# Kernel tuning notes

Measured on AMD Instinct MI355X. Metric: run time of the kernel, lower is better.

Reference implementation:

```python
import jax, jax.numpy as jnp
import numpy as np

P = 2.0  # exponent from init kwarg p


def _segment_mean(vals, idx, n):
    # scatter-mean with zero for empty segments (matches torch_scatter reduce='mean')
    s = jax.ops.segment_sum(vals, idx, num_segments=n)
    c = jax.ops.segment_sum(jnp.ones((vals.shape[0], 1), vals.dtype), idx, num_segments=n)
    return s / jnp.maximum(c, 1.0)


def setup_inputs() -> dict:
    key = jax.random.key(0)
    ks = jax.random.split(key, 6)
    N, E, nhid, heads = 100000, 3200000, 64, 4
    X = jax.random.normal(ks[0], (N, nhid), dtype=jnp.float32)
    edge_index = jax.random.randint(ks[1], (2, E), 0, N, dtype=jnp.int32)
    s1 = 1.0 / np.sqrt(nhid)
    W_self = jax.random.normal(ks[2], (nhid, nhid), dtype=jnp.float32) * s1
    W_neigh = jax.random.normal(ks[3], (nhid, nhid), dtype=jnp.float32) * s1
    b_conv = jnp.zeros((nhid,), dtype=jnp.float32)
    s2 = 1.0 / np.sqrt(2 * nhid)
    Qw = jax.random.normal(ks[4], (heads, 2 * nhid, nhid // heads), dtype=jnp.float32) * s2
    Qb = jnp.zeros((heads, nhid // heads), dtype=jnp.float32)
    return {"X": X, "edge_index": edge_index, "W_self": W_self,
            "W_neigh": W_neigh, "b_conv": b_conv, "Qw": Qw, "Qb": Qb}


def reference(X, edge_index, W_self, W_neigh, b_conv, Qw, Qb):
    N = X.shape[0]
    src, dst = edge_index[0], edge_index[1]
    # GraphSAGE conv: self-linear + linear over mean of neighbor features, then ReLU
    agg = _segment_mean(X[src], dst, N)                     # [N, nhid]
    X2 = jax.nn.relu(X @ W_self + agg @ W_neigh + b_conv)   # [N, nhid]
    # gather both edge endpoints and concat
    ef = jnp.concatenate([X2[src], X2[dst]], axis=1)        # [E, 2*nhid]
    # per-head small linear, abs^p, heads concatenated -> [E, nhid]
    h = jnp.einsum('ef,hfd->ehd', ef, Qw) + Qb              # [E, heads, nhid/heads]
    h = (jnp.abs(h) ** P).reshape(ef.shape[0], -1)
    # scatter-mean by source node, tanh
    gg = jnp.tanh(_segment_mean(h, src, N))                 # [N, nhid]
    return gg
```

## Files before the change

### kernel.cpp

```cpp
#include <hip/hip_runtime.h>
#include <math.h>

#define NHID 64
#define NPB 512
#define NPB_SHIFT 9
#define MAXB 256
#define CAP 20480
#define CHUNK 8192

__device__ __forceinline__ float bf_lo(unsigned u) { return __uint_as_float(u << 16); }
__device__ __forceinline__ float bf_hi(unsigned u) { return __uint_as_float(u & 0xffff0000u); }
__device__ __forceinline__ unsigned f2bf(float f) {
    unsigned u = __float_as_uint(f);
    return (u + 0x7fffu + ((u >> 16) & 1u)) >> 16;
}

__global__ __launch_bounds__(256) void k_build(const int* __restrict__ src,
                                               const int* __restrict__ dst,
                                               unsigned int* __restrict__ buf0,
                                               unsigned int* __restrict__ buf1,
                                               int* __restrict__ btail0,
                                               int* __restrict__ btail1,
                                               const float* __restrict__ X,
                                               unsigned* __restrict__ Xb,
                                               const float* __restrict__ Qw,
                                               float* __restrict__ W2,
                                               int E, int nB, int nBucketBlocks,
                                               int nXcastBlocks, int N) {
    __shared__ int h[MAXB], b[MAXB];
    __shared__ int sk[CHUNK];
    int bid = blockIdx.x;
    int tid = threadIdx.x;

    if (bid >= nBucketBlocks) {
        int xb = bid - nBucketBlocks;
        if (xb < nXcastBlocks) {
            int i = xb * 256 + tid;
            if (i < N * 8) {
                const float4* Xv = (const float4*)X;
                float4 f0 = Xv[(size_t)i * 2];
                float4 f1 = Xv[(size_t)i * 2 + 1];
                uint4 p;
                p.x = f2bf(f0.x) | (f2bf(f0.y) << 16);
                p.y = f2bf(f0.z) | (f2bf(f0.w) << 16);
                p.z = f2bf(f1.x) | (f2bf(f1.y) << 16);
                p.w = f2bf(f1.z) | (f2bf(f1.w) << 16);
                ((uint4*)Xb)[i] = p;
            }
        } else {
            int i = (xb - nXcastBlocks) * 256 + tid;
            if (i < 8192) {
                int f = i >> 7, c = i & 127;
                float v;
                if (c < 64) v = Qw[(c >> 4) * 2048 + f * 16 + (c & 15)];
                else { int cc = c - 64; v = Qw[(cc >> 4) * 2048 + (64 + f) * 16 + (cc & 15)]; }
                W2[i] = v;
            }
        }
        return;
    }

    int side  = bid & 1;
    int chunk = bid >> 1;
    const int* key = side ? src : dst;
    const int* pay = side ? dst : src;
    unsigned int* buf = side ? buf1 : buf0;
    int* btail = side ? btail1 : btail0;

    for (int i = tid; i < nB; i += 256) h[i] = 0;
    __syncthreads();
    int e0 = chunk * CHUNK;
    for (int i = tid; i < CHUNK / 4; i += 256) {
        int e = e0 + i * 4;
        int4 k4;
        if (e + 3 < E) {
            k4 = ((const int4*)(key + e0))[i];
            atomicAdd(&h[k4.x >> NPB_SHIFT], 1);
            atomicAdd(&h[k4.y >> NPB_SHIFT], 1);
            atomicAdd(&h[k4.z >> NPB_SHIFT], 1);
            atomicAdd(&h[k4.w >> NPB_SHIFT], 1);
        } else {
            k4.x = (e     < E) ? key[e]     : 0;
            k4.y = (e + 1 < E) ? key[e + 1] : 0;
            k4.z = (e + 2 < E) ? key[e + 2] : 0;
            k4.w = (e + 3 < E) ? key[e + 3] : 0;
            if (e     < E) atomicAdd(&h[k4.x >> NPB_SHIFT], 1);
            if (e + 1 < E) atomicAdd(&h[k4.y >> NPB_SHIFT], 1);
            if (e + 2 < E) atomicAdd(&h[k4.z >> NPB_SHIFT], 1);
            if (e + 3 < E) atomicAdd(&h[k4.w >> NPB_SHIFT], 1);
        }
        ((int4*)sk)[i] = k4;
    }
    __syncthreads();
    for (int i = tid; i < nB; i += 256) {
        int c = h[i];
        b[i] = c ? atomicAdd(&btail[i], c) : 0;
        h[i] = 0;
    }
    __syncthreads();
    for (int i = tid; i < CHUNK / 4; i += 256) {
        int e = e0 + i * 4;
        int4 k4 = ((const int4*)sk)[i];
        if (e + 3 < E) {
            int4 p4 = ((const int4*)(pay + e0))[i];
            int bb, r;
            bb = k4.x >> NPB_SHIFT; r = atomicAdd(&h[bb], 1) + b[bb];
            if (r < CAP) buf[(size_t)bb * CAP + r] = ((unsigned)p4.x << NPB_SHIFT) | (unsigned)(k4.x & (NPB - 1));
            bb = k4.y >> NPB_SHIFT; r = atomicAdd(&h[bb], 1) + b[bb];
            if (r < CAP) buf[(size_t)bb * CAP + r] = ((unsigned)p4.y << NPB_SHIFT) | (unsigned)(k4.y & (NPB - 1));
            bb = k4.z >> NPB_SHIFT; r = atomicAdd(&h[bb], 1) + b[bb];
            if (r < CAP) buf[(size_t)bb * CAP + r] = ((unsigned)p4.z << NPB_SHIFT) | (unsigned)(k4.z & (NPB - 1));
            bb = k4.w >> NPB_SHIFT; r = atomicAdd(&h[bb], 1) + b[bb];
            if (r < CAP) buf[(size_t)bb * CAP + r] = ((unsigned)p4.w << NPB_SHIFT) | (unsigned)(k4.w & (NPB - 1));
        } else {
            int ks[4] = {k4.x, k4.y, k4.z, k4.w};
            for (int j = 0; j < 4; ++j) {
                int e2 = e + j;
                if (e2 < E) {
                    int k = ks[j], p = pay[e2];
                    int bb = k >> NPB_SHIFT;
                    int r = atomicAdd(&h[bb], 1) + b[bb];
                    if (r < CAP) buf[(size_t)bb * CAP + r] = ((unsigned)p << NPB_SHIFT) | (unsigned)(k & (NPB - 1));
                }
            }
        }
    }
}

__global__ __launch_bounds__(256) void k_bscan(const int* __restrict__ btail0,
                                               const int* __restrict__ btail1,
                                               int* __restrict__ boff0, int* __restrict__ boff1,
                                               int* __restrict__ off0, int* __restrict__ off1,
                                               int nB, int N) {
    __shared__ int sd[256];
    int tid = threadIdx.x;
    int v = (tid < nB) ? min(btail0[tid], CAP) : 0;
    sd[tid] = v; __syncthreads();
    for (int o = 1; o < 256; o <<= 1) {
        int t = (tid >= o) ? sd[tid - o] : 0; __syncthreads();
        sd[tid] += t; __syncthreads();
    }
    if (tid < nB) boff0[tid] = sd[tid] - v;
    if (tid == 255) off0[N] = sd[255];
    __syncthreads();
    v = (tid < nB) ? min(btail1[tid], CAP) : 0;
    sd[tid] = v; __syncthreads();
    for (int o = 1; o < 256; o <<= 1) {
        int t = (tid >= o) ? sd[tid - o] : 0; __syncthreads();
        sd[tid] += t; __syncthreads();
    }
    if (tid < nB) boff1[tid] = sd[tid] - v;
    if (tid == 255) off1[N] = sd[255];
}

__device__ void csr_work(const unsigned int* __restrict__ bufb, int cnt_b, int boff,
                         int* __restrict__ off, int* __restrict__ csr,
                         int N, int bucket) {
    __shared__ int cnt[NPB];
    __shared__ int scn[NPB];
    __shared__ int cur[NPB];
    int tid = threadIdx.x;
    cnt[tid] = 0;
    __syncthreads();
    for (int i = tid; i < cnt_b; i += 512)
        atomicAdd(&cnt[bufb[i] & (NPB - 1)], 1);
    __syncthreads();
    int v = cnt[tid];
    scn[tid] = v; __syncthreads();
    for (int o = 1; o < 512; o <<= 1) {
        int t = (tid >= o) ? scn[tid - o] : 0; __syncthreads();
        scn[tid] += t; __syncthreads();
    }
    int base = boff + scn[tid] - v;
    cur[tid] = base;
    int node = (bucket << NPB_SHIFT) + tid;
    if (node < N) off[node] = base;
    __syncthreads();
    for (int i = tid; i < cnt_b; i += 512) {
        unsigned int u = bufb[i];
        int pos = atomicAdd(&cur[u & (NPB - 1)], 1);
        csr[pos] = (int)(u >> NPB_SHIFT);
    }
}

__global__ __launch_bounds__(512) void k_csr0(const unsigned int* __restrict__ buf0,
                                              const int* __restrict__ btail0,
                                              const int* __restrict__ boff0,
                                              int* __restrict__ off0,
                                              int* __restrict__ csr0, int N) {
    int b = blockIdx.x;
    csr_work(buf0 + (size_t)b * CAP, min(btail0[b], CAP), boff0[b], off0, csr0, N, b);
}

#define AGG_ACC(u) \
    accA.x += bf_lo(u.x); accA.y += bf_hi(u.x); \
    accA.z += bf_lo(u.y); accA.w += bf_hi(u.y); \
    accB.x += bf_lo(u.z); accB.y += bf_hi(u.z); \
    accB.z += bf_lo(u.w); accB.w += bf_hi(u.w);
#define AGG_ACCM(u, f) \
    accA.x += f * bf_lo(u.x); accA.y += f * bf_hi(u.x); \
    accA.z += f * bf_lo(u.y); accA.w += f * bf_hi(u.y); \
    accB.x += f * bf_lo(u.z); accB.y += f * bf_hi(u.z); \
    accB.z += f * bf_lo(u.w); accB.w += f * bf_hi(u.w);

__global__ __launch_bounds__(512) void k_aggcsr(const unsigned* __restrict__ Xb,
                                                const int* __restrict__ off_dst,
                                                const int* __restrict__ csr_dst,
                                                unsigned* __restrict__ aggb,
                                                const unsigned int* __restrict__ buf1,
                                                const int* __restrict__ btail1,
                                                const int* __restrict__ boff1,
                                                int* __restrict__ off1,
                                                int* __restrict__ csr1,
                                                int N, int nB) {
    int bid = blockIdx.x;
    if (bid < nB) {
        csr_work(buf1 + (size_t)bid * CAP, min(btail1[bid], CAP), boff1[bid],
                 off1, csr1, N, bid);
        return;
    }
    int abid = bid - nB;
    int tid = threadIdx.x;
    int lane = tid & 63;
    int node = abid * 8 + (tid >> 6);
    if (node >= N) return;
    int grp = lane >> 3, col8 = lane & 7;
    const uint4* Xb4 = (const uint4*)Xb;
    int s0 = off_dst[node], s1 = off_dst[node + 1];
    float4 accA = make_float4(0.f, 0.f, 0.f, 0.f);
    float4 accB = make_float4(0.f, 0.f, 0.f, 0.f);
    for (int base = s0; base < s1; base += 64) {
        int cnt = min(64, s1 - base);
        int idx = (base + lane < s1) ? csr_dst[base + lane] : 0;
        int j = 0;
        for (; j + 32 <= cnt; j += 32) {
            int m0 = __shfl(idx, j + grp);
            int m1 = __shfl(idx, j + 8 + grp);
            int m2 = __shfl(idx, j + 16 + grp);
            int m3 = __shfl(idx, j + 24 + grp);
            uint4 u0 = Xb4[(size_t)m0 * 8 + col8];
            uint4 u1 = Xb4[(size_t)m1 * 8 + col8];
            uint4 u2 = Xb4[(size_t)m2 * 8 + col8];
            uint4 u3 = Xb4[(size_t)m3 * 8 + col8];
            AGG_ACC(u0); AGG_ACC(u1); AGG_ACC(u2); AGG_ACC(u3);
        }
        if (j < cnt) {
            int q0 = j + grp, q1 = j + 8 + grp, q2 = j + 16 + grp, q3 = j + 24 + grp;
            int m0 = __shfl(idx, q0);
            int m1 = __shfl(idx, q1);
            int m2 = __shfl(idx, q2);
            int m3 = __shfl(idx, q3);
            float f0 = (q0 < cnt) ? 1.f : 0.f; if (q0 >= cnt) m0 = 0;
            float f1 = (q1 < cnt) ? 1.f : 0.f; if (q1 >= cnt) m1 = 0;
            float f2 = (q2 < cnt) ? 1.f : 0.f; if (q2 >= cnt) m2 = 0;
            float f3 = (q3 < cnt) ? 1.f : 0.f; if (q3 >= cnt) m3 = 0;
            uint4 u0 = Xb4[(size_t)m0 * 8 + col8];
            uint4 u1 = Xb4[(size_t)m1 * 8 + col8];
            uint4 u2 = Xb4[(size_t)m2 * 8 + col8];
            uint4 u3 = Xb4[(size_t)m3 * 8 + col8];
            AGG_ACCM(u0, f0); AGG_ACCM(u1, f1); AGG_ACCM(u2, f2); AGG_ACCM(u3, f3);
        }
    }
    #pragma unroll
    for (int d = 8; d < 64; d <<= 1) {
        accA.x += __shfl_xor(accA.x, d); accA.y += __shfl_xor(accA.y, d);
        accA.z += __shfl_xor(accA.z, d); accA.w += __shfl_xor(accA.w, d);
        accB.x += __shfl_xor(accB.x, d); accB.y += __shfl_xor(accB.y, d);
        accB.z += __shfl_xor(accB.z, d); accB.w += __shfl_xor(accB.w, d);
    }
    if (grp == 0) {
        int deg = s1 - s0;
        float inv = 1.f / (float)max(deg, 1);
        uint4 p;
        p.x = f2bf(accA.x * inv) | (f2bf(accA.y * inv) << 16);
        p.y = f2bf(accA.z * inv) | (f2bf(accA.w * inv) << 16);
        p.z = f2bf(accB.x * inv) | (f2bf(accB.y * inv) << 16);
        p.w = f2bf(accB.z * inv) | (f2bf(accB.w * inv) << 16);
        ((uint4*)aggb)[(size_t)node * 8 + col8] = p;
    }
}

__global__ __launch_bounds__(256) void k_phaseA(const unsigned* __restrict__ Xb,
                                                const unsigned* __restrict__ aggb,
                                                const float* __restrict__ Ws,
                                                const float* __restrict__ Wn,
                                                const float* __restrict__ bconv,
                                                unsigned* __restrict__ X2b, int N) {
    __shared__ float sWs[4096];
    __shared__ float sWn[4096];
    __shared__ float sb[64];
    int tid = threadIdx.x;
    for (int i = tid; i < 4096; i += 256) {
        sWs[i] = Ws[i];
        sWn[i] = Wn[i];
    }
    if (tid < 64) sb[tid] = bconv[tid];
    __syncthreads();

    int n = blockIdx.x * 64 + (tid >> 2);
    if (n >= N) return;
    int wb = (tid & 3) << 2;
    const float4* ws4 = (const float4*)sWs;
    const float4* wn4 = (const float4*)sWn;
    const float4* bv  = (const float4*)sb;
    const uint4* Xv  = (const uint4*)Xb + (size_t)n * 8;
    const uint4* Gv  = (const uint4*)aggb + (size_t)n * 8;
    float4 a0 = bv[wb], a1 = bv[wb + 1], a2 = bv[wb + 2], a3 = bv[wb + 3];
    #pragma unroll 2
    for (int q8 = 0; q8 < 8; ++q8) {
        uint4 xu = Xv[q8];
        uint4 gu = Gv[q8];
        float xs[8] = {bf_lo(xu.x), bf_hi(xu.x), bf_lo(xu.y), bf_hi(xu.y),
                       bf_lo(xu.z), bf_hi(xu.z), bf_lo(xu.w), bf_hi(xu.w)};
        float gs[8] = {bf_lo(gu.x), bf_hi(gu.x), bf_lo(gu.y), bf_hi(gu.y),
                       bf_lo(gu.z), bf_hi(gu.z), bf_lo(gu.w), bf_hi(gu.w)};
        #pragma unroll
        for (int j = 0; j < 8; ++j) {
            int k16 = (8 * q8 + j) * 16 + wb;
            float4 w0 = ws4[k16], w1 = ws4[k16 + 1], w2 = ws4[k16 + 2], w3 = ws4[k16 + 3];
            float4 m0 = wn4[k16], m1 = wn4[k16 + 1], m2 = wn4[k16 + 2], m3 = wn4[k16 + 3];
            float xj = xs[j], gj = gs[j];
            a0.x += xj * w0.x + gj * m0.x; a0.y += xj * w0.y + gj * m0.y;
            a0.z += xj * w0.z + gj * m0.z; a0.w += xj * w0.w + gj * m0.w;
            a1.x += xj * w1.x + gj * m1.x; a1.y += xj * w1.y + gj * m1.y;
            a1.z += xj * w1.z + gj * m1.z; a1.w += xj * w1.w + gj * m1.w;
            a2.x += xj * w2.x + gj * m2.x; a2.y += xj * w2.y + gj * m2.y;
            a2.z += xj * w2.z + gj * m2.z; a2.w += xj * w2.w + gj * m2.w;
            a3.x += xj * w3.x + gj * m3.x; a3.y += xj * w3.y + gj * m3.y;
            a3.z += xj * w3.z + gj * m3.z; a3.w += xj * w3.w + gj * m3.w;
        }
    }
    a0.x = fmaxf(a0.x, 0.f); a0.y = fmaxf(a0.y, 0.f); a0.z = fmaxf(a0.z, 0.f); a0.w = fmaxf(a0.w, 0.f);
    a1.x = fmaxf(a1.x, 0.f); a1.y = fmaxf(a1.y, 0.f); a1.z = fmaxf(a1.z, 0.f); a1.w = fmaxf(a1.w, 0.f);
    a2.x = fmaxf(a2.x, 0.f); a2.y = fmaxf(a2.y, 0.f); a2.z = fmaxf(a2.z, 0.f); a2.w = fmaxf(a2.w, 0.f);
    a3.x = fmaxf(a3.x, 0.f); a3.y = fmaxf(a3.y, 0.f); a3.z = fmaxf(a3.z, 0.f); a3.w = fmaxf(a3.w, 0.f);
    uint4 p0, p1;
    p0.x = f2bf(a0.x) | (f2bf(a0.y) << 16);
    p0.y = f2bf(a0.z) | (f2bf(a0.w) << 16);
    p0.z = f2bf(a1.x) | (f2bf(a1.y) << 16);
    p0.w = f2bf(a1.z) | (f2bf(a1.w) << 16);
    p1.x = f2bf(a2.x) | (f2bf(a2.y) << 16);
    p1.y = f2bf(a2.z) | (f2bf(a2.w) << 16);
    p1.z = f2bf(a3.x) | (f2bf(a3.y) << 16);
    p1.w = f2bf(a3.z) | (f2bf(a3.w) << 16);
    uint4* outp = (uint4*)X2b + (size_t)n * 8 + (tid & 3) * 2;
    outp[0] = p0; outp[1] = p1;
}

__global__ __launch_bounds__(256) void k_phaseB(const unsigned* __restrict__ X2b,
                                                const float* __restrict__ W2,
                                                const float* __restrict__ Qb,
                                                unsigned* __restrict__ aOut,
                                                unsigned* __restrict__ bOut, int N) {
    __shared__ float sW[10240];
    int tid = threadIdx.x;
    for (int i = tid; i < 8192; i += 256) {
        int f = i >> 7, c = i & 127;
        sW[f * 160 + (c >> 4) * 20 + (c & 15)] = W2[i];
    }
    __syncthreads();

    int n = blockIdx.x * 32 + (tid >> 3);
    if (n >= N) return;
    int part = tid & 7;
    const float4* w4 = (const float4*)sW;
    float4 a0, a1, a2, a3;
    if (part < 4) {
        const float4* qv = (const float4*)Qb;
        int wb = part << 2;
        a0 = qv[wb]; a1 = qv[wb + 1]; a2 = qv[wb + 2]; a3 = qv[wb + 3];
    } else {
        a0 = a1 = a2 = a3 = make_float4(0.f, 0.f, 0.f, 0.f);
    }
    const uint4* Xv = (const uint4*)X2b + (size_t)n * 8;
    int pbase = part * 5;
    #pragma unroll 2
    for (int q8 = 0; q8 < 8; ++q8) {
        uint4 xu = Xv[q8];
        float xs[8] = {bf_lo(xu.x), bf_hi(xu.x), bf_lo(xu.y), bf_hi(xu.y),
                       bf_lo(xu.z), bf_hi(xu.z), bf_lo(xu.w), bf_hi(xu.w)};
        #pragma unroll
        for (int j = 0; j < 8; ++j) {
            int b4 = (8 * q8 + j) * 40 + pbase;
            float4 w0 = w4[b4], w1 = w4[b4 + 1], w2 = w4[b4 + 2], w3 = w4[b4 + 3];
            float xj = xs[j];
            a0.x += xj * w0.x; a0.y += xj * w0.y; a0.z += xj * w0.z; a0.w += xj * w0.w;
            a1.x += xj * w1.x; a1.y += xj * w1.y; a1.z += xj * w1.z; a1.w += xj * w1.w;
            a2.x += xj * w2.x; a2.y += xj * w2.y; a2.z += xj * w2.z; a2.w += xj * w2.w;
            a3.x += xj * w3.x; a3.y += xj * w3.y; a3.z += xj * w3.z; a3.w += xj * w3.w;
        }
    }
    uint4 p0, p1;
    p0.x = f2bf(a0.x) | (f2bf(a0.y) << 16);
    p0.y = f2bf(a0.z) | (f2bf(a0.w) << 16);
    p0.z = f2bf(a1.x) | (f2bf(a1.y) << 16);
    p0.w = f2bf(a1.z) | (f2bf(a1.w) << 16);
    p1.x = f2bf(a2.x) | (f2bf(a2.y) << 16);
    p1.y = f2bf(a2.z) | (f2bf(a2.w) << 16);
    p1.z = f2bf(a3.x) | (f2bf(a3.y) << 16);
    p1.w = f2bf(a3.z) | (f2bf(a3.w) << 16);
    uint4* outp = (part < 4) ? (uint4*)aOut + (size_t)n * 8 + part * 2
                             : (uint4*)bOut + (size_t)n * 8 + (part - 4) * 2;
    outp[0] = p0; outp[1] = p1;
}

#define FIN_ACC(u) { float t; \
    t = avA.x + bf_lo(u.x); accA.x += t * t; \
    t = avA.y + bf_hi(u.x); accA.y += t * t; \
    t = avA.z + bf_lo(u.y); accA.z += t * t; \
    t = avA.w + bf_hi(u.y); accA.w += t * t; \
    t = avB.x + bf_lo(u.z); accB.x += t * t; \
    t = avB.y + bf_hi(u.z); accB.y += t * t; \
    t = avB.z + bf_lo(u.w); accB.z += t * t; \
    t = avB.w + bf_hi(u.w); accB.w += t * t; }
#define FIN_ACCM(u, f) { float t; \
    t = avA.x + bf_lo(u.x); accA.x += f * t * t; \
    t = avA.y + bf_hi(u.x); accA.y += f * t * t; \
    t = avA.z + bf_lo(u.y); accA.z += f * t * t; \
    t = avA.w + bf_hi(u.y); accA.w += f * t * t; \
    t = avB.x + bf_lo(u.z); accB.x += f * t * t; \
    t = avB.y + bf_hi(u.z); accB.y += f * t * t; \
    t = avB.z + bf_lo(u.w); accB.z += f * t * t; \
    t = avB.w + bf_hi(u.w); accB.w += f * t * t; }

__global__ __launch_bounds__(256) void k_final(const unsigned* __restrict__ aFb,
                                               const unsigned* __restrict__ bFb,
                                               const int* __restrict__ off_src,
                                               const int* __restrict__ csr_src,
                                               float* __restrict__ out, int N) {
    int lane = threadIdx.x & 63;
    int node = blockIdx.x * 4 + (threadIdx.x >> 6);
    if (node >= N) return;
    int grp = lane >> 3, col8 = lane & 7;
    const uint4* Bv = (const uint4*)bFb;
    uint4 au = ((const uint4*)aFb)[(size_t)node * 8 + col8];
    float4 avA = make_float4(bf_lo(au.x), bf_hi(au.x), bf_lo(au.y), bf_hi(au.y));
    float4 avB = make_float4(bf_lo(au.z), bf_hi(au.z), bf_lo(au.w), bf_hi(au.w));
    int s0 = off_src[node], s1 = off_src[node + 1];
    float4 accA = make_float4(0.f, 0.f, 0.f, 0.f);
    float4 accB = make_float4(0.f, 0.f, 0.f, 0.f);
    for (int base = s0; base < s1; base += 64) {
        int cnt = min(64, s1 - base);
        int idx = (base + lane < s1) ? csr_src[base + lane] : 0;
        int j = 0;
        for (; j + 32 <= cnt; j += 32) {
            int m0 = __shfl(idx, j + grp);
            int m1 = __shfl(idx, j + 8 + grp);
            int m2 = __shfl(idx, j + 16 + grp);
            int m3 = __shfl(idx, j + 24 + grp);
            uint4 u0 = Bv[(size_t)m0 * 8 + col8];
            uint4 u1 = Bv[(size_t)m1 * 8 + col8];
            uint4 u2 = Bv[(size_t)m2 * 8 + col8];
            uint4 u3 = Bv[(size_t)m3 * 8 + col8];
            FIN_ACC(u0); FIN_ACC(u1); FIN_ACC(u2); FIN_ACC(u3);
        }
        if (j < cnt) {
            int q0 = j + grp, q1 = j + 8 + grp, q2 = j + 16 + grp, q3 = j + 24 + grp;
            int m0 = __shfl(idx, q0);
            int m1 = __shfl(idx, q1);
            int m2 = __shfl(idx, q2);
            int m3 = __shfl(idx, q3);
            float f0 = (q0 < cnt) ? 1.f : 0.f; if (q0 >= cnt) m0 = 0;
            float f1 = (q1 < cnt) ? 1.f : 0.f; if (q1 >= cnt) m1 = 0;
            float f2 = (q2 < cnt) ? 1.f : 0.f; if (q2 >= cnt) m2 = 0;
            float f3 = (q3 < cnt) ? 1.f : 0.f; if (q3 >= cnt) m3 = 0;
            uint4 u0 = Bv[(size_t)m0 * 8 + col8];
            uint4 u1 = Bv[(size_t)m1 * 8 + col8];
            uint4 u2 = Bv[(size_t)m2 * 8 + col8];
            uint4 u3 = Bv[(size_t)m3 * 8 + col8];
            FIN_ACCM(u0, f0); FIN_ACCM(u1, f1); FIN_ACCM(u2, f2); FIN_ACCM(u3, f3);
        }
    }
    #pragma unroll
    for (int d = 8; d < 64; d <<= 1) {
        accA.x += __shfl_xor(accA.x, d); accA.y += __shfl_xor(accA.y, d);
        accA.z += __shfl_xor(accA.z, d); accA.w += __shfl_xor(accA.w, d);
        accB.x += __shfl_xor(accB.x, d); accB.y += __shfl_xor(accB.y, d);
        accB.z += __shfl_xor(accB.z, d); accB.w += __shfl_xor(accB.w, d);
    }
    if (grp == 0) {
        int deg = s1 - s0;
        float inv = 1.f / (float)max(deg, 1);
        float4 r0 = make_float4(tanhf(accA.x * inv), tanhf(accA.y * inv),
                                tanhf(accA.z * inv), tanhf(accA.w * inv));
        float4 r1 = make_float4(tanhf(accB.x * inv), tanhf(accB.y * inv),
                                tanhf(accB.z * inv), tanhf(accB.w * inv));
        ((float4*)out)[(size_t)node * 16 + col8 * 2]     = r0;
        ((float4*)out)[(size_t)node * 16 + col8 * 2 + 1] = r1;
    }
}

extern "C" void kernel_launch(void* const* d_in, const int* in_sizes, int n_in,
                              void* d_out, int out_size, void* d_ws, size_t ws_size,
                              hipStream_t stream) {
    const float* X      = (const float*)d_in[0];
    const int*   ei     = (const int*)d_in[1];
    const float* Wself  = (const float*)d_in[2];
    const float* Wneigh = (const float*)d_in[3];
    const float* bconv  = (const float*)d_in[4];
    const float* Qw     = (const float*)d_in[5];
    const float* Qb     = (const float*)d_in[6];

    int N = in_sizes[0] / NHID;
    int E = in_sizes[1] / 2;
    const int* src = ei;
    const int* dst = ei + E;
    int nB = (N + NPB - 1) >> NPB_SHIFT;
    int nChunks = (E + CHUNK - 1) / CHUNK;

    char* ws = (char*)d_ws;
    size_t bufBytes = (size_t)MAXB * CAP * 4;
    size_t NH2 = (size_t)N * NHID * 2;
    unsigned int* buf0 = (unsigned int*)(ws);
    unsigned int* buf1 = (unsigned int*)(ws + bufBytes);
    unsigned* X2b  = (unsigned*)(ws);
    unsigned* aFb  = (unsigned*)(ws + NH2);
    unsigned* bFb  = (unsigned*)(ws + 2 * NH2);
    unsigned* Xb   = (unsigned*)(ws + 2 * bufBytes);
    unsigned* aggb = (unsigned*)(ws + 2 * bufBytes + NH2);
    size_t pos = 2 * bufBytes + 2 * NH2;
    pos = (pos + 255) & ~(size_t)255;
    auto alloc = [&](size_t bytes) -> void* {
        void* p = ws + pos;
        pos = (pos + bytes + 255) & ~(size_t)255;
        return p;
    };
    int* csr0   = (int*)alloc((size_t)E * 4);
    int* csr1   = (int*)alloc((size_t)E * 4);
    int* off0   = (int*)alloc((size_t)(N + 1) * 4);
    int* off1   = (int*)alloc((size_t)(N + 1) * 4);
    int* btail0 = (int*)alloc((size_t)MAXB * 4);
    int* btail1 = (int*)alloc((size_t)MAXB * 4);
    int* boff0  = (int*)alloc((size_t)MAXB * 4);
    int* boff1  = (int*)alloc((size_t)MAXB * 4);
    float* W2   = (float*)alloc((size_t)8192 * 4);
    (void)ws_size; (void)n_in; (void)out_size;

    hipMemsetAsync(btail0, 0, (size_t)2 * MAXB * 4, stream);

    int nBucketBlocks = nChunks * 2;
    int nXcastBlocks  = (N * 8 + 255) / 256;
    int nBuildBlocks  = nBucketBlocks + nXcastBlocks + 32;
    int aggBlocks     = (N + 7) / 8;

    k_build<<<nBuildBlocks, 256, 0, stream>>>(src, dst, buf0, buf1, btail0, btail1,
                                              X, Xb, Qw, W2,
                                              E, nB, nBucketBlocks, nXcastBlocks, N);
    k_bscan<<<1, 256, 0, stream>>>(btail0, btail1, boff0, boff1, off0, off1, nB, N);
    k_csr0<<<nB, 512, 0, stream>>>(buf0, btail0, boff0, off0, csr0, N);
    k_aggcsr<<<nB + aggBlocks, 512, 0, stream>>>(Xb, off0, csr0, aggb,
                                                 buf1, btail1, boff1, off1, csr1,
                                                 N, nB);
    k_phaseA<<<(N + 63) / 64, 256, 0, stream>>>(Xb, aggb, Wself, Wneigh, bconv, X2b, N);
    k_phaseB<<<(N + 31) / 32, 256, 0, stream>>>(X2b, W2, Qb, aFb, bFb, N);
    k_final<<<(N + 3) / 4, 256, 0, stream>>>(aFb, bFb, off1, csr1, (float*)d_out, N);
}
```

Baseline: 318.6 us.

## Fuse bucket scan into CSR kernels and merge phase A/B linears

Removes the single-block k_bscan launch: each CSR block now computes its own bucket base offset with a prefix scan over all bucket tails. It also fuses the SAGE linear (phase A) with the per-head projection (phase B), keeping X2 in shared memory rather than writing it to global memory and reading it back. This saves two kernel launches and a global round trip of the N×64 bf16 intermediate. In exchange, every CSR block repeats the bucket scan, and the fused kernel uses more shared memory (about 90KB), which may lower occupancy.

```diff
diff --git a/kernel.cpp b/kernel.cpp
--- a/kernel.cpp
+++ b/kernel.cpp
@@ -127,50 +127,35 @@
     }
 }
 
-__global__ __launch_bounds__(256) void k_bscan(const int* __restrict__ btail0,
-                                               const int* __restrict__ btail1,
-                                               int* __restrict__ boff0, int* __restrict__ boff1,
-                                               int* __restrict__ off0, int* __restrict__ off1,
-                                               int nB, int N) {
-    __shared__ int sd[256];
-    int tid = threadIdx.x;
-    int v = (tid < nB) ? min(btail0[tid], CAP) : 0;
-    sd[tid] = v; __syncthreads();
-    for (int o = 1; o < 256; o <<= 1) {
-        int t = (tid >= o) ? sd[tid - o] : 0; __syncthreads();
-        sd[tid] += t; __syncthreads();
-    }
-    if (tid < nB) boff0[tid] = sd[tid] - v;
-    if (tid == 255) off0[N] = sd[255];
-    __syncthreads();
-    v = (tid < nB) ? min(btail1[tid], CAP) : 0;
-    sd[tid] = v; __syncthreads();
-    for (int o = 1; o < 256; o <<= 1) {
-        int t = (tid >= o) ? sd[tid - o] : 0; __syncthreads();
-        sd[tid] += t; __syncthreads();
-    }
-    if (tid < nB) boff1[tid] = sd[tid] - v;
-    if (tid == 255) off1[N] = sd[255];
-}
-
-__device__ void csr_work(const unsigned int* __restrict__ bufb, int cnt_b, int boff,
+__device__ void csr_work(const unsigned int* __restrict__ bufb,
+                         const int* __restrict__ btail, int nB,
                          int* __restrict__ off, int* __restrict__ csr,
                          int N, int bucket) {
     __shared__ int cnt[NPB];
     __shared__ int scn[NPB];
     __shared__ int cur[NPB];
     int tid = threadIdx.x;
-    cnt[tid] = 0;
-    __syncthreads();
-    for (int i = tid; i < cnt_b; i += 512)
-        atomicAdd(&cnt[bufb[i] & (NPB - 1)], 1);
-    __syncthreads();
-    int v = cnt[tid];
+    int v = (tid < nB && tid < bucket) ? min(btail[tid], CAP) : 0;
     scn[tid] = v; __syncthreads();
     for (int o = 1; o < 512; o <<= 1) {
         int t = (tid >= o) ? scn[tid - o] : 0; __syncthreads();
         scn[tid] += t; __syncthreads();
     }
+    int boff = scn[511];
+    int cnt_b = min(btail[bucket], CAP);
+    if (bucket == nB - 1 && tid == 0) off[N] = boff + cnt_b;
+    __syncthreads();
+    cnt[tid] = 0;
+    __syncthreads();
+    for (int i = tid; i < cnt_b; i += 512)
+        atomicAdd(&cnt[bufb[i] & (NPB - 1)], 1);
+    __syncthreads();
+    v = cnt[tid];
+    scn[tid] = v; __syncthreads();
+    for (int o = 1; o < 512; o <<= 1) {
+        int t = (tid >= o) ? scn[tid - o] : 0; __syncthreads();
+        scn[tid] += t; __syncthreads();
+    }
     int base = boff + scn[tid] - v;
     cur[tid] = base;
     int node = (bucket << NPB_SHIFT) + tid;
@@ -185,11 +170,10 @@
 
 __global__ __launch_bounds__(512) void k_csr0(const unsigned int* __restrict__ buf0,
                                               const int* __restrict__ btail0,
-                                              const int* __restrict__ boff0,
                                               int* __restrict__ off0,
-                                              int* __restrict__ csr0, int N) {
+                                              int* __restrict__ csr0, int N, int nB) {
     int b = blockIdx.x;
-    csr_work(buf0 + (size_t)b * CAP, min(btail0[b], CAP), boff0[b], off0, csr0, N, b);
+    csr_work(buf0 + (size_t)b * CAP, btail0, nB, off0, csr0, N, b);
 }
 
 #define AGG_ACC(u) \
@@ -209,14 +193,12 @@
                                                 unsigned* __restrict__ aggb,
                                                 const unsigned int* __restrict__ buf1,
                                                 const int* __restrict__ btail1,
-                                                const int* __restrict__ boff1,
                                                 int* __restrict__ off1,
                                                 int* __restrict__ csr1,
                                                 int N, int nB) {
     int bid = blockIdx.x;
     if (bid < nB) {
-        csr_work(buf1 + (size_t)bid * CAP, min(btail1[bid], CAP), boff1[bid],
-                 off1, csr1, N, bid);
+        csr_work(buf1 + (size_t)bid * CAP, btail1, nB, off1, csr1, N, bid);
         return;
     }
     int abid = bid - nB;
@@ -280,128 +262,116 @@
     }
 }
 
-__global__ __launch_bounds__(256) void k_phaseA(const unsigned* __restrict__ Xb,
-                                                const unsigned* __restrict__ aggb,
-                                                const float* __restrict__ Ws,
-                                                const float* __restrict__ Wn,
-                                                const float* __restrict__ bconv,
-                                                unsigned* __restrict__ X2b, int N) {
+__global__ __launch_bounds__(256) void k_phaseAB(const unsigned* __restrict__ Xb,
+                                                 const unsigned* __restrict__ aggb,
+                                                 const float* __restrict__ Ws,
+                                                 const float* __restrict__ Wn,
+                                                 const float* __restrict__ bconv,
+                                                 const float* __restrict__ W2,
+                                                 const float* __restrict__ Qb,
+                                                 unsigned* __restrict__ aOut,
+                                                 unsigned* __restrict__ bOut, int N) {
     __shared__ float sWs[4096];
     __shared__ float sWn[4096];
+    __shared__ float sW2[10240];
     __shared__ float sb[64];
+    __shared__ unsigned sX2[32 * 36];
     int tid = threadIdx.x;
-    for (int i = tid; i < 4096; i += 256) {
-        sWs[i] = Ws[i];
-        sWn[i] = Wn[i];
-    }
-    if (tid < 64) sb[tid] = bconv[tid];
-    __syncthreads();
-
-    int n = blockIdx.x * 64 + (tid >> 2);
-    if (n >= N) return;
-    int wb = (tid & 3) << 2;
-    const float4* ws4 = (const float4*)sWs;
-    const float4* wn4 = (const float4*)sWn;
-    const float4* bv  = (const float4*)sb;
-    const uint4* Xv  = (const uint4*)Xb + (size_t)n * 8;
-    const uint4* Gv  = (const uint4*)aggb + (size_t)n * 8;
-    float4 a0 = bv[wb], a1 = bv[wb + 1], a2 = bv[wb + 2], a3 = bv[wb + 3];
-    #pragma unroll 2
-    for (int q8 = 0; q8 < 8; ++q8) {
-        uint4 xu = Xv[q8];
-        uint4 gu = Gv[q8];
-        float xs[8] = {bf_lo(xu.x), bf_hi(xu.x), bf_lo(xu.y), bf_hi(xu.y),
-                       bf_lo(xu.z), bf_hi(xu.z), bf_lo(xu.w), bf_hi(xu.w)};
-        float gs[8] = {bf_lo(gu.x), bf_hi(gu.x), bf_lo(gu.y), bf_hi(gu.y),
-                       bf_lo(gu.z), bf_hi(gu.z), bf_lo(gu.w), bf_hi(gu.w)};
-        #pragma unroll
-        for (int j = 0; j < 8; ++j) {
-            int k16 = (8 * q8 + j) * 16 + wb;
-            float4 w0 = ws4[k16], w1 = ws4[k16 + 1], w2 = ws4[k16 + 2], w3 = ws4[k16 + 3];
-            float4 m0 = wn4[k16], m1 = wn4[k16 + 1], m2 = wn4[k16 + 2], m3 = wn4[k16 + 3];
-            float xj = xs[j], gj = gs[j];
-            a0.x += xj * w0.x + gj * m0.x; a0.y += xj * w0.y + gj * m0.y;
-            a0.z += xj * w0.z + gj * m0.z; a0.w += xj * w0.w + gj * m0.w;
-            a1.x += xj * w1.x + gj * m1.x; a1.y += xj * w1.y + gj * m1.y;
-            a1.z += xj * w1.z + gj * m1.z; a1.w += xj * w1.w + gj * m1.w;
-            a2.x += xj * w2.x + gj * m2.x; a2.y += xj * w2.y + gj * m2.y;
-            a2.z += xj * w2.z + gj * m2.z; a2.w += xj * w2.w + gj * m2.w;
-            a3.x += xj * w3.x + gj * m3.x; a3.y += xj * w3.y + gj * m3.y;
-            a3.z += xj * w3.z + gj * m3.z; a3.w += xj * w3.w + gj * m3.w;
-        }
-    }
-    a0.x = fmaxf(a0.x, 0.f); a0.y = fmaxf(a0.y, 0.f); a0.z = fmaxf(a0.z, 0.f); a0.w = fmaxf(a0.w, 0.f);
-    a1.x = fmaxf(a1.x, 0.f); a1.y = fmaxf(a1.y, 0.f); a1.z = fmaxf(a1.z, 0.f); a1.w = fmaxf(a1.w, 0.f);
-    a2.x = fmaxf(a2.x, 0.f); a2.y = fmaxf(a2.y, 0.f); a2.z = fmaxf(a2.z, 0.f); a2.w = fmaxf(a2.w, 0.f);
-    a3.x = fmaxf(a3.x, 0.f); a3.y = fmaxf(a3.y, 0.f); a3.z = fmaxf(a3.z, 0.f); a3.w = fmaxf(a3.w, 0.f);
-    uint4 p0, p1;
-    p0.x = f2bf(a0.x) | (f2bf(a0.y) << 16);
-    p0.y = f2bf(a0.z) | (f2bf(a0.w) << 16);
-    p0.z = f2bf(a1.x) | (f2bf(a1.y) << 16);
-    p0.w = f2bf(a1.z) | (f2bf(a1.w) << 16);
-    p1.x = f2bf(a2.x) | (f2bf(a2.y) << 16);
-    p1.y = f2bf(a2.z) | (f2bf(a2.w) << 16);
-    p1.z = f2bf(a3.x) | (f2bf(a3.y) << 16);
-    p1.w = f2bf(a3.z) | (f2bf(a3.w) << 16);
-    uint4* outp = (uint4*)X2b + (size_t)n * 8 + (tid & 3) * 2;
-    outp[0] = p0; outp[1] = p1;
-}
-
-__global__ __launch_bounds__(256) void k_phaseB(const unsigned* __restrict__ X2b,
-                                                const float* __restrict__ W2,
-                                                const float* __restrict__ Qb,
-                                                unsigned* __restrict__ aOut,
-                                                unsigned* __restrict__ bOut, int N) {
-    __shared__ float sW[10240];
-    int tid = threadIdx.x;
+    for (int i = tid; i < 4096; i += 256) { sWs[i] = Ws[i]; sWn[i] = Wn[i]; }
     for (int i = tid; i < 8192; i += 256) {
         int f = i >> 7, c = i & 127;
-        sW[f * 160 + (c >> 4) * 20 + (c & 15)] = W2[i];
-    }
-    __syncthreads();
-
-    int n = blockIdx.x * 32 + (tid >> 3);
-    if (n >= N) return;
+        sW2[f * 160 + (c >> 4) * 20 + (c & 15)] = W2[i];
+    }
+    if (tid < 64) sb[tid] = bconv[tid];
+    __syncthreads();
+
+    int nl = tid >> 3;
+    int n = blockIdx.x * 32 + nl;
     int part = tid & 7;
-    const float4* w4 = (const float4*)sW;
-    float4 a0, a1, a2, a3;
-    if (part < 4) {
-        const float4* qv = (const float4*)Qb;
-        int wb = part << 2;
-        a0 = qv[wb]; a1 = qv[wb + 1]; a2 = qv[wb + 2]; a3 = qv[wb + 3];
-    } else {
-        a0 = a1 = a2 = a3 = make_float4(0.f, 0.f, 0.f, 0.f);
-    }
-    const uint4* Xv = (const uint4*)X2b + (size_t)n * 8;
-    int pbase = part * 5;
-    #pragma unroll 2
-    for (int q8 = 0; q8 < 8; ++q8) {
-        uint4 xu = Xv[q8];
-        float xs[8] = {bf_lo(xu.x), bf_hi(xu.x), bf_lo(xu.y), bf_hi(xu.y),
-                       bf_lo(xu.z), bf_hi(xu.z), bf_lo(xu.w), bf_hi(xu.w)};
-        #pragma unroll
-        for (int j = 0; j < 8; ++j) {
-            int b4 = (8 * q8 + j) * 40 + pbase;
-            float4 w0 = w4[b4], w1 = w4[b4 + 1], w2 = w4[b4 + 2], w3 = w4[b4 + 3];
-            float xj = xs[j];
-            a0.x += xj * w0.x; a0.y += xj * w0.y; a0.z += xj * w0.z; a0.w += xj * w0.w;
-            a1.x += xj * w1.x; a1.y += xj * w1.y; a1.z += xj * w1.z; a1.w += xj * w1.w;
-            a2.x += xj * w2.x; a2.y += xj * w2.y; a2.z += xj * w2.z; a2.w += xj * w2.w;
-            a3.x += xj * w3.x; a3.y += xj * w3.y; a3.z += xj * w3.z; a3.w += xj * w3.w;
-        }
-    }
-    uint4 p0, p1;
-    p0.x = f2bf(a0.x) | (f2bf(a0.y) << 16);
-    p0.y = f2bf(a0.z) | (f2bf(a0.w) << 16);
-    p0.z = f2bf(a1.x) | (f2bf(a1.y) << 16);
-    p0.w = f2bf(a1.z) | (f2bf(a1.w) << 16);
-    p1.x = f2bf(a2.x) | (f2bf(a2.y) << 16);
-    p1.y = f2bf(a2.z) | (f2bf(a2.w) << 16);
-    p1.z = f2bf(a3.x) | (f2bf(a3.y) << 16);
-    p1.w = f2bf(a3.z) | (f2bf(a3.w) << 16);
-    uint4* outp = (part < 4) ? (uint4*)aOut + (size_t)n * 8 + part * 2
-                             : (uint4*)bOut + (size_t)n * 8 + (part - 4) * 2;
-    outp[0] = p0; outp[1] = p1;
+    bool valid = (n < N);
+
+    if (valid) {
+        const uint4* Xv = (const uint4*)Xb + (size_t)n * 8;
+        const uint4* Gv = (const uint4*)aggb + (size_t)n * 8;
+        int cb = part * 2;
+        const float4* ws4 = (const float4*)sWs;
+        const float4* wn4 = (const float4*)sWn;
+        const float4* bv  = (const float4*)sb;
+        float4 a0 = bv[cb], a1 = bv[cb + 1];
+        #pragma unroll 2
+        for (int q8 = 0; q8 < 8; ++q8) {
+            uint4 xu = Xv[q8];
+            uint4 gu = Gv[q8];
+            float xs[8] = {bf_lo(xu.x), bf_hi(xu.x), bf_lo(xu.y), bf_hi(xu.y),
+                           bf_lo(xu.z), bf_hi(xu.z), bf_lo(xu.w), bf_hi(xu.w)};
+            float gs[8] = {bf_lo(gu.x), bf_hi(gu.x), bf_lo(gu.y), bf_hi(gu.y),
+                           bf_lo(gu.z), bf_hi(gu.z), bf_lo(gu.w), bf_hi(gu.w)};
+            #pragma unroll
+            for (int j = 0; j < 8; ++j) {
+                int k16 = (8 * q8 + j) * 16 + cb;
+                float4 w0 = ws4[k16], w1 = ws4[k16 + 1];
+                float4 m0 = wn4[k16], m1 = wn4[k16 + 1];
+                float xj = xs[j], gj = gs[j];
+                a0.x += xj * w0.x + gj * m0.x; a0.y += xj * w0.y + gj * m0.y;
+                a0.z += xj * w0.z + gj * m0.z; a0.w += xj * w0.w + gj * m0.w;
+                a1.x += xj * w1.x + gj * m1.x; a1.y += xj * w1.y + gj * m1.y;
+                a1.z += xj * w1.z + gj * m1.z; a1.w += xj * w1.w + gj * m1.w;
+            }
+        }
+        a0.x = fmaxf(a0.x, 0.f); a0.y = fmaxf(a0.y, 0.f);
+        a0.z = fmaxf(a0.z, 0.f); a0.w = fmaxf(a0.w, 0.f);
+        a1.x = fmaxf(a1.x, 0.f); a1.y = fmaxf(a1.y, 0.f);
+        a1.z = fmaxf(a1.z, 0.f); a1.w = fmaxf(a1.w, 0.f);
+        uint4 p;
+        p.x = f2bf(a0.x) | (f2bf(a0.y) << 16);
+        p.y = f2bf(a0.z) | (f2bf(a0.w) << 16);
+        p.z = f2bf(a1.x) | (f2bf(a1.y) << 16);
+        p.w = f2bf(a1.z) | (f2bf(a1.w) << 16);
+        *((uint4*)(sX2 + nl * 36 + part * 4)) = p;
+    }
+    __syncthreads();
+
+    if (valid) {
+        const float4* w4 = (const float4*)sW2;
+        float4 a0, a1, a2, a3;
+        if (part < 4) {
+            const float4* qv = (const float4*)Qb;
+            int wb = part << 2;
+            a0 = qv[wb]; a1 = qv[wb + 1]; a2 = qv[wb + 2]; a3 = qv[wb + 3];
+        } else {
+            a0 = a1 = a2 = a3 = make_float4(0.f, 0.f, 0.f, 0.f);
+        }
+        const uint4* Xv2 = (const uint4*)(sX2 + nl * 36);
+        int pbase = part * 5;
+        #pragma unroll 2
+        for (int q8 = 0; q8 < 8; ++q8) {
+            uint4 xu = Xv2[q8];
+            float xs[8] = {bf_lo(xu.x), bf_hi(xu.x), bf_lo(xu.y), bf_hi(xu.y),
+                           bf_lo(xu.z), bf_hi(xu.z), bf_lo(xu.w), bf_hi(xu.w)};
+            #pragma unroll
+            for (int j = 0; j < 8; ++j) {
+                int b4 = (8 * q8 + j) * 40 + pbase;
+                float4 w0 = w4[b4], w1 = w4[b4 + 1], w2 = w4[b4 + 2], w3 = w4[b4 + 3];
+                float xj = xs[j];
+                a0.x += xj * w0.x; a0.y += xj * w0.y; a0.z += xj * w0.z; a0.w += xj * w0.w;
+                a1.x += xj * w1.x; a1.y += xj * w1.y; a1.z += xj * w1.z; a1.w += xj * w1.w;
+                a2.x += xj * w2.x; a2.y += xj * w2.y; a2.z += xj * w2.z; a2.w += xj * w2.w;
+                a3.x += xj * w3.x; a3.y += xj * w3.y; a3.z += xj * w3.z; a3.w += xj * w3.w;
+            }
+        }
+        uint4 p0, p1;
+        p0.x = f2bf(a0.x) | (f2bf(a0.y) << 16);
+        p0.y = f2bf(a0.z) | (f2bf(a0.w) << 16);
+        p0.z = f2bf(a1.x) | (f2bf(a1.y) << 16);
+        p0.w = f2bf(a1.z) | (f2bf(a1.w) << 16);
+        p1.x = f2bf(a2.x) | (f2bf(a2.y) << 16);
+        p1.y = f2bf(a2.z) | (f2bf(a2.w) << 16);
+        p1.z = f2bf(a3.x) | (f2bf(a3.y) << 16);
+        p1.w = f2bf(a3.z) | (f2bf(a3.w) << 16);
+        uint4* outp = (part < 4) ? (uint4*)aOut + (size_t)n * 8 + part * 2
+                                 : (uint4*)bOut + (size_t)n * 8 + (part - 4) * 2;
+        outp[0] = p0; outp[1] = p1;
+    }
 }
 
 #define FIN_ACC(u) { float t; \
@@ -513,9 +483,8 @@
     size_t NH2 = (size_t)N * NHID * 2;
     unsigned int* buf0 = (unsigned int*)(ws);
     unsigned int* buf1 = (unsigned int*)(ws + bufBytes);
-    unsigned* X2b  = (unsigned*)(ws);
-    unsigned* aFb  = (unsigned*)(ws + NH2);
-    unsigned* bFb  = (unsigned*)(ws + 2 * NH2);
+    unsigned* aFb  = (unsigned*)(ws);
+    unsigned* bFb  = (unsigned*)(ws + NH2);
     unsigned* Xb   = (unsigned*)(ws + 2 * bufBytes);
     unsigned* aggb = (unsigned*)(ws + 2 * bufBytes + NH2);
     size_t pos = 2 * bufBytes + 2 * NH2;
@@ -531,8 +500,6 @@
     int* off1   = (int*)alloc((size_t)(N + 1) * 4);
     int* btail0 = (int*)alloc((size_t)MAXB * 4);
     int* btail1 = (int*)alloc((size_t)MAXB * 4);
-    int* boff0  = (int*)alloc((size_t)MAXB * 4);
-    int* boff1  = (int*)alloc((size_t)MAXB * 4);
     float* W2   = (float*)alloc((size_t)8192 * 4);
     (void)ws_size; (void)n_in; (void)out_size;
 
@@ -546,12 +513,11 @@
     k_build<<<nBuildBlocks, 256, 0, stream>>>(src, dst, buf0, buf1, btail0, btail1,
                                               X, Xb, Qw, W2,
                                               E, nB, nBucketBlocks, nXcastBlocks, N);
-    k_bscan<<<1, 256, 0, stream>>>(btail0, btail1, boff0, boff1, off0, off1, nB, N);
-    k_csr0<<<nB, 512, 0, stream>>>(buf0, btail0, boff0, off0, csr0, N);
+    k_csr0<<<nB, 512, 0, stream>>>(buf0, btail0, off0, csr0, N, nB);
     k_aggcsr<<<nB + aggBlocks, 512, 0, stream>>>(Xb, off0, csr0, aggb,
-                                                 buf1, btail1, boff1, off1, csr1,
+                                                 buf1, btail1, off1, csr1,
                                                  N, nB);
-    k_phaseA<<<(N + 63) / 64, 256, 0, stream>>>(Xb, aggb, Wself, Wneigh, bconv, X2b, N);
-    k_phaseB<<<(N + 31) / 32, 256, 0, stream>>>(X2b, W2, Qb, aFb, bFb, N);
+    k_phaseAB<<<(N + 31) / 32, 256, 0, stream>>>(Xb, aggb, Wself, Wneigh, bconv,
+                                                 W2, Qb, aFb, bFb, N);
     k_final<<<(N + 3) / 4, 256, 0, stream>>>(aFb, bFb, off1, csr1, (float*)d_out, N);
 }
```

New measurement: 369.2 us. 1.16x slower.
